# Optimization experiments

Hardware: AMD Instinct MI355X
Metric: run time of the kernel (lower is better)

Reference implementation:

```python
import jax, jax.numpy as jnp
import numpy as np

B, L, D, H, MEM, POL = 32, 256, 768, 12, 384, 3
DK = D // H
ALPHA, BETA, GAMA = 1.0, 0.25, 0.1


def _forward(sequence_output, pooled_output, adj_reshape, src_mask, aspect_mask,
             ln_g, ln_b, wq, bq, wk, bk, wd, bd, weight_m, bias_m,
             wa0, ba0, wa1, ba1, ws0, bs0, ws1, bs1, affine1, affine2, wc, bc):
    b, l, d = sequence_output.shape
    h = weight_m.shape[0]
    dk = d // h

    # custom LayerNorm (torch std is unbiased, ddof=1)
    mu = sequence_output.mean(-1, keepdims=True)
    sd = jnp.std(sequence_output, axis=-1, keepdims=True, ddof=1)
    x = ln_g * (sequence_output - mu) / (sd + 1e-6) + ln_b  # gcn_inputs (dropout = eval identity)

    aspect_outs = x * aspect_mask[:, :, None]

    # multi-head projections  [B,H,L,dk]
    q = (x @ wq + bq).reshape(b, l, h, dk).transpose(0, 2, 1, 3)
    k = (x @ wk + bk).reshape(b, l, h, dk).transpose(0, 2, 1, 3)
    asp = aspect_outs @ wd + bd                       # [B,L,dk]
    asp = jnp.broadcast_to(asp[:, None], (b, h, l, dk))

    # aspect-conditioned scores: tanh(aspect @ W_m @ K^T + b_m)   [B,H,L,L]
    asps = jnp.tanh(jnp.einsum('bhld,hde,bhme->bhlm', asp, weight_m, k) + bias_m[0])
    avg = asps.sum(axis=-2) / l                       # [B,H,L]

    # fusion overwrite: for each aspect index idx, row idx and col idx <- avg.
    # Sequential loop semantics (ascending idx, row-then-col) collapse to:
    #   both aspect (i,j): value = avg[min(i,j)];  row-only: avg[j];  col-only: avg[i]
    is_asp = aspect_mask > 0                          # [B,L]
    rowm = is_asp[:, None, :, None]
    colm = is_asp[:, None, None, :]
    avg_i = avg[..., :, None]                         # [B,H,L,1]
    avg_j = avg[..., None, :]                         # [B,H,1,L]
    ge = (jnp.arange(l)[:, None] >= jnp.arange(l)[None, :])  # i>=j -> min=j
    both_val = jnp.where(ge, avg_j, avg_i)
    aspect_scores = jnp.where(rowm & colm, both_val,
                      jnp.where(rowm, avg_j,
                        jnp.where(colm, avg_i, asps)))

    # standard scaled-dot attention
    scores = jnp.einsum('bhld,bhmd->bhlm', q, k) / jnp.sqrt(jnp.float32(dk))
    scores = jnp.where(src_mask[:, None, None, :] == 0, -1e9, scores)
    s_attn = jax.nn.softmax(scores, axis=-1)          # dropout = eval identity

    aspect_score_avg = aspect_scores.mean(axis=1)     # [B,L,L]
    adj_s = s_attn.mean(axis=1)                       # [B,L,L]

    eye = jnp.eye(l, dtype=adj_s.dtype)
    adj_s = adj_s * (1.0 - eye) + eye                 # zero diag then add identity
    adj_s = src_mask[:, :, None] * adj_s

    adj_r = jnp.exp(ALPHA * adj_reshape)
    dist_mask = aspect_score_avg > BETA
    adj_r = jnp.where(dist_mask, 1.0, adj_r)
    adj_ag = adj_r * aspect_score_avg

    log_p = jax.nn.log_softmax(adj_ag, axis=-1)
    log_q = jax.nn.log_softmax(adj_s, axis=-1)
    q_t = jnp.exp(log_q)
    kl = jnp.sum(q_t * (log_q - log_p))
    kl_loss = jnp.exp(-1.0 * kl * GAMA)

    denom_s = adj_s.sum(axis=2, keepdims=True) + 1.0
    denom_ag = adj_ag.sum(axis=2, keepdims=True) + 1.0

    out_ag, out_s = x, x
    was = [(wa0, ba0), (wa1, ba1)]
    wss = [(ws0, bs0), (ws1, bs1)]
    for li in range(2):
        g_ag = jax.nn.relu(((adj_ag @ out_ag) @ was[li][0] + was[li][1]) / denom_ag)
        g_s = jax.nn.relu(((adj_s @ out_s) @ wss[li][0] + wss[li][1]) / denom_s)
        A1 = jax.nn.softmax(jnp.einsum('bld,de,bme->blm', g_ag, affine1, g_s), axis=-1)
        A2 = jax.nn.softmax(jnp.einsum('bld,de,bme->blm', g_s, affine2, g_ag), axis=-1)
        out_ag = A1 @ g_s
        out_s = A2 @ g_ag   # gcn_drop = eval identity

    asp_wn = aspect_mask.sum(axis=1, keepdims=True)   # [B,1]
    m = aspect_mask[:, :, None]
    outputs1 = (out_ag * m).sum(axis=1) / asp_wn      # [B,MEM]
    outputs2 = (out_s * m).sum(axis=1) / asp_wn

    final = jnp.concatenate([outputs1, outputs2, pooled_output], axis=-1) @ wc + bc
    return final, kl_loss


def setup_inputs() -> dict:
    key = jax.random.key(0)
    ks = jax.random.split(key, 16)
    s = 0.02
    pos = jnp.arange(L)
    start = 5 + (jnp.arange(B) % 16)
    aspect_mask = ((pos[None, :] >= start[:, None]) & (pos[None, :] < start[:, None] + 3)).astype(jnp.float32)
    f32 = jnp.float32
    return {
        'sequence_output': jax.random.normal(ks[0], (B, L, D), f32),
        'pooled_output': jax.random.normal(ks[1], (B, D), f32),
        'adj_reshape': jax.random.uniform(ks[2], (B, L, L), f32),
        'src_mask': jnp.ones((B, L), f32),
        'aspect_mask': aspect_mask,
        'ln_g': jnp.ones((D,), f32), 'ln_b': jnp.zeros((D,), f32),
        'wq': jax.random.normal(ks[3], (D, D), f32) * s, 'bq': jnp.zeros((D,), f32),
        'wk': jax.random.normal(ks[4], (D, D), f32) * s, 'bk': jnp.zeros((D,), f32),
        'wd': jax.random.normal(ks[5], (D, DK), f32) * s, 'bd': jnp.zeros((DK,), f32),
        'weight_m': jax.random.normal(ks[6], (H, DK, DK), f32) * s,
        'bias_m': jnp.zeros((1,), f32),
        'wa0': jax.random.normal(ks[7], (D, MEM), f32) * s, 'ba0': jnp.zeros((MEM,), f32),
        'wa1': jax.random.normal(ks[8], (MEM, MEM), f32) * s, 'ba1': jnp.zeros((MEM,), f32),
        'ws0': jax.random.normal(ks[9], (D, MEM), f32) * s, 'bs0': jnp.zeros((MEM,), f32),
        'ws1': jax.random.normal(ks[10], (MEM, MEM), f32) * s, 'bs1': jnp.zeros((MEM,), f32),
        'affine1': jax.random.normal(ks[11], (MEM, MEM), f32) * s,
        'affine2': jax.random.normal(ks[12], (MEM, MEM), f32) * s,
        'wc': jax.random.normal(ks[13], (2 * D, POL), f32) * s, 'bc': jnp.zeros((POL,), f32),
    }


def reference(sequence_output, pooled_output, adj_reshape, src_mask, aspect_mask,
              ln_g, ln_b, wq, bq, wk, bk, wd, bd, weight_m, bias_m,
              wa0, ba0, wa1, ba1, ws0, bs0, ws1, bs1, affine1, affine2, wc, bc):
    return _forward(sequence_output, pooled_output, adj_reshape, src_mask, aspect_mask,
                    ln_g, ln_b, wq, bq, wk, bk, wd, bd, weight_m, bias_m,
                    wa0, ba0, wa1, ba1, ws0, bs0, ws1, bs1, affine1, affine2, wc, bc)
```

## Files before the change

### kernel.cpp

```cpp
#include <hip/hip_runtime.h>

#define B_ 32
#define L_ 256
#define D_ 768
#define H_ 12
#define DK_ 64
#define MEM_ 384

typedef __attribute__((ext_vector_type(8))) short bfrag8;
typedef __attribute__((ext_vector_type(8))) unsigned short us8;
typedef __attribute__((ext_vector_type(4))) float f32x4;

__device__ inline unsigned short f2bf(float f) {
  unsigned u = __float_as_uint(f);
  return (unsigned short)((u + 0x7fffu + ((u >> 16) & 1u)) >> 16);
}
__device__ inline float bf2f(unsigned short u) {
  return __uint_as_float(((unsigned)u) << 16);
}
__device__ inline float tanh_fast(float x) {
  x = fminf(fmaxf(x, -30.f), 30.f);
  float e = __expf(2.f * x);
  return (e - 1.f) * __builtin_amdgcn_rcpf(e + 1.f);
}
__device__ inline void gload_lds16(const unsigned short* g, unsigned short* l) {
  __builtin_amdgcn_global_load_lds(
      (__attribute__((address_space(1))) void*)(g),
      (__attribute__((address_space(3))) void*)(l), 16, 0, 0);
}

__device__ inline float waveRedSum(float v) {
#pragma unroll
  for (int o = 32; o; o >>= 1) v += __shfl_xor(v, o, 64);
  return v;
}
__device__ inline float waveRedMax(float v) {
#pragma unroll
  for (int o = 32; o; o >>= 1) v = fmaxf(v, __shfl_xor(v, o, 64));
  return v;
}
__device__ inline float blkRedSum(float v, float* red) {
  v = waveRedSum(v);
  int w = threadIdx.x >> 6;
  __syncthreads();
  if ((threadIdx.x & 63) == 0) red[w] = v;
  __syncthreads();
  return red[0] + red[1] + red[2] + red[3];
}
__device__ inline float blkRedMax(float v, float* red) {
  v = waveRedMax(v);
  int w = threadIdx.x >> 6;
  __syncthreads();
  if ((threadIdx.x & 63) == 0) red[w] = v;
  __syncthreads();
  return fmaxf(fmaxf(red[0], red[1]), fmaxf(red[2], red[3]));
}

__global__ __launch_bounds__(256) void prep_kernel(
    const float* __restrict__ seq, const float* __restrict__ lng,
    const float* __restrict__ lnb, float* __restrict__ xout,
    unsigned short* __restrict__ xbf,
    const float* __restrict__ wq, unsigned short* __restrict__ wqT,
    const float* __restrict__ wk, unsigned short* __restrict__ wkT,
    const float* __restrict__ wa0, unsigned short* __restrict__ wa0T,
    const float* __restrict__ ws0, unsigned short* __restrict__ ws0T,
    const float* __restrict__ wa1, unsigned short* __restrict__ wa1T,
    const float* __restrict__ ws1, unsigned short* __restrict__ ws1T,
    const float* __restrict__ aff1, unsigned short* __restrict__ aff1T,
    const float* __restrict__ aff2, unsigned short* __restrict__ aff2T,
    const float* __restrict__ wd, unsigned short* __restrict__ wdT,
    const float* __restrict__ wm, unsigned short* __restrict__ wmT) {
  int bid = blockIdx.x;
  if (bid >= 600) {
    long row = bid - 600;
    const float* p = seq + row * D_;
    float v[3];
#pragma unroll
    for (int i = 0; i < 3; ++i) v[i] = p[threadIdx.x + i * 256];
    __shared__ float red[4];
    float s = v[0] + v[1] + v[2];
    s = blkRedSum(s, red);
    float mu = s * (1.f / D_);
    float ss = 0.f;
#pragma unroll
    for (int i = 0; i < 3; ++i) { float d = v[i] - mu; ss += d * d; }
    ss = blkRedSum(ss, red);
    float sd = sqrtf(ss * (1.f / (D_ - 1)));
    float inv = 1.f / (sd + 1e-6f);
#pragma unroll
    for (int i = 0; i < 3; ++i) {
      int c = threadIdx.x + i * 256;
      float o = lng[c] * (v[i] - mu) * inv + lnb[c];
      xout[row * D_ + c] = o;
      xbf[row * D_ + c] = f2bf(o);
    }
    return;
  }
  const float* src; unsigned short* dst; int Rr, Cc, tIdx;
  if (bid < 144)      { src = wq;   dst = wqT;   Rr = 768; Cc = 768; tIdx = bid; }
  else if (bid < 288) { src = wk;   dst = wkT;   Rr = 768; Cc = 768; tIdx = bid - 144; }
  else if (bid < 360) { src = wa0;  dst = wa0T;  Rr = 768; Cc = 384; tIdx = bid - 288; }
  else if (bid < 432) { src = ws0;  dst = ws0T;  Rr = 768; Cc = 384; tIdx = bid - 360; }
  else if (bid < 468) { src = wa1;  dst = wa1T;  Rr = 384; Cc = 384; tIdx = bid - 432; }
  else if (bid < 504) { src = ws1;  dst = ws1T;  Rr = 384; Cc = 384; tIdx = bid - 468; }
  else if (bid < 540) { src = aff1; dst = aff1T; Rr = 384; Cc = 384; tIdx = bid - 504; }
  else if (bid < 576) { src = aff2; dst = aff2T; Rr = 384; Cc = 384; tIdx = bid - 540; }
  else if (bid < 588) { src = wd;   dst = wdT;   Rr = 768; Cc = 64;  tIdx = bid - 576; }
  else { int h = bid - 588; src = wm + h * 4096; dst = wmT + h * 4096; Rr = 64; Cc = 64; tIdx = 0; }
  __shared__ float tile[64][65];
  int nx = Cc >> 6;
  int c0 = (tIdx % nx) * 64, r0 = (tIdx / nx) * 64;
  int tx = threadIdx.x & 63, ty = threadIdx.x >> 6;
#pragma unroll
  for (int i = 0; i < 16; ++i)
    tile[ty + i * 4][tx] = src[(long)(r0 + ty + i * 4) * Cc + c0 + tx];
  __syncthreads();
#pragma unroll
  for (int i = 0; i < 16; ++i)
    dst[(long)(c0 + ty + i * 4) * Rr + r0 + tx] = f2bf(tile[tx][ty + i * 4]);
}

template <int MR>
__global__ __launch_bounds__(256) void gemm_bb(
    const unsigned short* __restrict__ A, const unsigned short* __restrict__ Bt,
    float* __restrict__ C, unsigned short* __restrict__ Cbf,
    unsigned short* __restrict__ CT,
    int M, int N, int K, long sA, long sB, long sC, long sCT,
    const float* __restrict__ bias, const float* __restrict__ rowDiv, int relu,
    const unsigned short* __restrict__ A2, const unsigned short* __restrict__ Bt2,
    float* __restrict__ C2, unsigned short* __restrict__ Cbf2,
    unsigned short* __restrict__ CT2,
    const float* __restrict__ bias2, const float* __restrict__ rowDiv2, int zsplit) {
  constexpr int MFRAG = MR / 32;
  constexpr int RW = MR / 2;
  constexpr int ASH = MR * 32;
  constexpr int BUFS = ASH + 4096;
  constexpr int TSH = 64 * (MR + 8);
  constexpr int SMN = (2 * BUFS > TSH) ? 2 * BUFS : TSH;
  __shared__ alignas(16) unsigned short smem[SMN];
  const int tid = threadIdx.x;
  const int bn = blockIdx.x, bm = blockIdx.y;
  int bz = blockIdx.z;
  const unsigned short* Ap = A; const unsigned short* Btp = Bt;
  float* Cp = C; unsigned short* Cbp = Cbf; unsigned short* CTp = CT;
  const float* biasp = bias; const float* rowDivp = rowDiv;
  if (zsplit > 0 && bz >= zsplit) {
    bz -= zsplit;
    Ap = A2; Btp = Bt2; Cp = C2; Cbp = Cbf2; CTp = CT2; biasp = bias2; rowDivp = rowDiv2;
  }
  Ap += (long)bz * sA; Btp += (long)bz * sB;
  if (Cp) Cp += (long)bz * sC;
  if (Cbp) Cbp += (long)bz * sC;
  if (CTp) CTp += (long)bz * sCT;

  f32x4 acc[MFRAG][4] = {};
  const int l = tid & 63, w = tid >> 6;
  const int wr = w >> 1, wc = w & 1;
  const int lr = l & 15, sg = l >> 4;

  const int rc = l >> 2;
  const int sslot = (l & 3) ^ ((rc >> 1) & 3);
  const unsigned short* gA0 = Ap + (long)(bm * MR + w * 16 + rc) * K + sslot * 8;
  const unsigned short* gA1 = (MR == 128)
      ? Ap + (long)(bm * MR + (w + 4) * 16 + rc) * K + sslot * 8 : nullptr;
  const unsigned short* gB0 = Btp + (long)(bn * 128 + w * 16 + rc) * K + sslot * 8;
  const unsigned short* gB1 = Btp + (long)(bn * 128 + (w + 4) * 16 + rc) * K + sslot * 8;
  const int stA0 = w * 512, stA1 = (w + 4) * 512;
  const int stB0 = ASH + w * 512, stB1 = ASH + (w + 4) * 512;

  const int swz = (sg ^ ((lr >> 1) & 3)) * 8;
  int aoff[MFRAG], boff[4];
#pragma unroll
  for (int m = 0; m < MFRAG; ++m) aoff[m] = (wr * RW + m * 16 + lr) * 32 + swz;
#pragma unroll
  for (int n = 0; n < 4; ++n) boff[n] = ASH + (wc * 64 + n * 16 + lr) * 32 + swz;

  const int nt = K >> 5;
  gload_lds16(gA0, smem + stA0);
  if (MR == 128) gload_lds16(gA1, smem + stA1);
  gload_lds16(gB0, smem + stB0);
  gload_lds16(gB1, smem + stB1);
  __syncthreads();

  for (int t = 0; t < nt; ++t) {
    const int cur = (t & 1) * BUFS;
    if (t + 1 < nt) {
      const int nxt = ((t + 1) & 1) * BUFS;
      const int k1 = (t + 1) << 5;
      gload_lds16(gA0 + k1, smem + nxt + stA0);
      if (MR == 128) gload_lds16(gA1 + k1, smem + nxt + stA1);
      gload_lds16(gB0 + k1, smem + nxt + stB0);
      gload_lds16(gB1 + k1, smem + nxt + stB1);
    }
    bfrag8 af[MFRAG], bf[4];
#pragma unroll
    for (int m = 0; m < MFRAG; ++m) af[m] = *(const bfrag8*)(smem + cur + aoff[m]);
#pragma unroll
    for (int n = 0; n < 4; ++n) bf[n] = *(const bfrag8*)(smem + cur + boff[n]);
#pragma unroll
    for (int m = 0; m < MFRAG; ++m)
#pragma unroll
      for (int n = 0; n < 4; ++n)
        acc[m][n] = __builtin_amdgcn_mfma_f32_16x16x32_bf16(af[m], bf[n], acc[m][n], 0, 0, 0);
    __syncthreads();
  }

  if (Cp || Cbp) {
#pragma unroll
    for (int m = 0; m < MFRAG; ++m) {
#pragma unroll
      for (int r = 0; r < 4; ++r) {
        int row = bm * MR + wr * RW + m * 16 + (l >> 4) * 4 + r;
        float rd = rowDivp ? 1.f / rowDivp[(long)bz * M + row] : 1.f;
#pragma unroll
        for (int n = 0; n < 4; ++n) {
          int col = bn * 128 + wc * 64 + n * 16 + lr;
          float v = acc[m][n][r];
          if (biasp) v += biasp[col];
          v *= rd;
          if (relu) v = fmaxf(v, 0.f);
          if (Cp) Cp[(long)row * N + col] = v;
          if (Cbp) Cbp[(long)row * N + col] = f2bf(v);
        }
      }
    }
  }
  if (CT) {
    auto Ts = (unsigned short(*)[MR + 8])smem;
#pragma unroll
    for (int ch = 0; ch < 2; ++ch) {
      __syncthreads();
      if (wc == ch) {
#pragma unroll
        for (int m = 0; m < MFRAG; ++m) {
#pragma unroll
          for (int r = 0; r < 4; ++r) {
            int rowl = wr * RW + m * 16 + (l >> 4) * 4 + r;
            float rd = rowDivp ? 1.f / rowDivp[(long)bz * M + bm * MR + rowl] : 1.f;
#pragma unroll
            for (int n = 0; n < 4; ++n) {
              int col = bn * 128 + wc * 64 + n * 16 + lr;
              float v = acc[m][n][r];
              if (biasp) v += biasp[col];
              v *= rd;
              if (relu) v = fmaxf(v, 0.f);
              Ts[n * 16 + lr][rowl] = f2bf(v);
            }
          }
        }
      }
      __syncthreads();
      int trow = tid >> 2, tc = (tid & 3) * (MR / 4);
      int colg = bn * 128 + ch * 64 + trow;
      int rowg = bm * MR + tc;
      unsigned short* dp = CTp + (long)(rowg >> 8) * sCT + (long)colg * 256 + (rowg & 255);
#pragma unroll
      for (int j = 0; j < MR / 32; ++j)
        *(us8*)(dp + j * 8) = *(const us8*)&Ts[trow][tc + j * 8];
    }
  }
}

__global__ __launch_bounds__(256) void attn_asp(
    const unsigned short* __restrict__ qbf, const unsigned short* __restrict__ kbf,
    const float* __restrict__ srcm,
    float* __restrict__ part0, float* __restrict__ part1,
    const unsigned short* __restrict__ xbf, const unsigned short* __restrict__ wdT,
    const float* __restrict__ amask, const float* __restrict__ bd,
    unsigned short* __restrict__ aspbf) {
  int t = threadIdx.x;
  int w = t >> 6, l = t & 63;
  int lr = l & 15, kg = (l >> 4) * 8;
  if (blockIdx.x >= 1024) {
    int l0 = (blockIdx.x - 1024) << 4;
    const unsigned short* ap = xbf + (long)(l0 + lr) * D_ + kg;
    const unsigned short* bp = wdT + (long)(w * 16 + lr) * D_ + kg;
    f32x4 acc = {};
#pragma unroll
    for (int k0 = 0; k0 < D_; k0 += 32) {
      bfrag8 af = *(const bfrag8*)(ap + k0);
      bfrag8 bf = *(const bfrag8*)(bp + k0);
      acc = __builtin_amdgcn_mfma_f32_16x16x32_bf16(af, bf, acc, 0, 0, 0);
    }
    int col = w * 16 + lr;
#pragma unroll
    for (int r = 0; r < 4; ++r) {
      int row = l0 + (l >> 4) * 4 + r;
      float v = acc[r] * amask[row] + bd[col];
      aspbf[(long)row * DK_ + col] = f2bf(v);
    }
    return;
  }
  int d = blockIdx.x;
  int b = (d & 7) + 8 * ((d >> 3) & 3);
  int rest = d >> 5;
  int l0 = (rest & 15) << 4;
  int half = rest >> 4;
  int rbase = (l >> 4) * 4;
  __shared__ float red[3][2][16][4];
  float acc[4][4] = {};
  float cmv[4];
#pragma unroll
  for (int ct = 0; ct < 4; ++ct) cmv[ct] = srcm[b * L_ + w * 64 + ct * 16 + lr];

#pragma unroll 1
  for (int ph = 0; ph < 3; ++ph) {
    int hp = half * 3 + ph;
    const unsigned short* ap = qbf + ((long)b * L_ + l0 + lr) * D_ + hp * 128 + kg;
    bfrag8 a00 = *(const bfrag8*)ap;
    bfrag8 a01 = *(const bfrag8*)(ap + 32);
    bfrag8 a10 = *(const bfrag8*)(ap + 64);
    bfrag8 a11 = *(const bfrag8*)(ap + 96);
    bfrag8 kv[4][4];
#pragma unroll
    for (int ct = 0; ct < 4; ++ct) {
      const unsigned short* bp =
          kbf + ((long)b * L_ + w * 64 + ct * 16 + lr) * D_ + hp * 128 + kg;
      kv[ct][0] = *(const bfrag8*)bp;
      kv[ct][1] = *(const bfrag8*)(bp + 32);
      kv[ct][2] = *(const bfrag8*)(bp + 64);
      kv[ct][3] = *(const bfrag8*)(bp + 96);
    }
    float sv0[4][4], sv1[4][4];
#pragma unroll
    for (int ct = 0; ct < 4; ++ct) {
      f32x4 c0 = {}, c1 = {};
      c0 = __builtin_amdgcn_mfma_f32_16x16x32_bf16(a00, kv[ct][0], c0, 0, 0, 0);
      c0 = __builtin_amdgcn_mfma_f32_16x16x32_bf16(a01, kv[ct][1], c0, 0, 0, 0);
      c1 = __builtin_amdgcn_mfma_f32_16x16x32_bf16(a10, kv[ct][2], c1, 0, 0, 0);
      c1 = __builtin_amdgcn_mfma_f32_16x16x32_bf16(a11, kv[ct][3], c1, 0, 0, 0);
      bool msk = (cmv[ct] == 0.f);
#pragma unroll
      for (int r = 0; r < 4; ++r) {
        sv0[ct][r] = __expf(msk ? -1e9f : c0[r] * 0.125f);
        sv1[ct][r] = __expf(msk ? -1e9f : c1[r] * 0.125f);
      }
    }
#pragma unroll
    for (int r = 0; r < 4; ++r) {
      float s0 = sv0[0][r] + sv0[1][r] + sv0[2][r] + sv0[3][r];
      float s1 = sv1[0][r] + sv1[1][r] + sv1[2][r] + sv1[3][r];
#pragma unroll
      for (int o = 1; o < 16; o <<= 1) {
        s0 += __shfl_xor(s0, o, 64);
        s1 += __shfl_xor(s1, o, 64);
      }
      if (lr == 0) {
        red[ph][0][rbase + r][w] = s0;
        red[ph][1][rbase + r][w] = s1;
      }
    }
    __syncthreads();
#pragma unroll
    for (int r = 0; r < 4; ++r) {
      f32x4 s4 = *(const f32x4*)&red[ph][0][rbase + r][0];
      float inv0 = __builtin_amdgcn_rcpf(s4[0] + s4[1] + s4[2] + s4[3] + 1e-30f);
      f32x4 t4 = *(const f32x4*)&red[ph][1][rbase + r][0];
      float inv1 = __builtin_amdgcn_rcpf(t4[0] + t4[1] + t4[2] + t4[3] + 1e-30f);
#pragma unroll
      for (int ct = 0; ct < 4; ++ct)
        acc[ct][r] += sv0[ct][r] * inv0 + sv1[ct][r] * inv1;
    }
  }

  float* pp = half ? part1 : part0;
#pragma unroll
  for (int r = 0; r < 4; ++r) {
    int row = l0 + rbase + r;
#pragma unroll
    for (int ct = 0; ct < 4; ++ct) {
      int col = w * 64 + ct * 16 + lr;
      pp[((long)b * L_ + row) * L_ + col] = acc[ct][r];
    }
  }
}

__global__ __launch_bounds__(256) void asp_wm_v2(const unsigned short* __restrict__ aspbf,
                                                 const unsigned short* __restrict__ wmT,
                                                 unsigned short* __restrict__ tmpA) {
  int bh = blockIdx.x;
  int b = bh / H_, h = bh % H_;
  int t = threadIdx.x;
  int w = t >> 6, l = t & 63;
  int lr = l & 15, kg = (l >> 4) * 8;
  const unsigned short* wp = wmT + h * 4096;
  f32x4 acc[4][4] = {};
#pragma unroll
  for (int ks = 0; ks < 2; ++ks) {
    int k0 = ks * 32;
    bfrag8 af[4], bf[4];
#pragma unroll
    for (int m = 0; m < 4; ++m)
      af[m] = *(const bfrag8*)(aspbf + (long)(b * L_ + w * 64 + m * 16 + lr) * DK_ + k0 + kg);
#pragma unroll
    for (int n = 0; n < 4; ++n)
      bf[n] = *(const bfrag8*)(wp + (n * 16 + lr) * 64 + k0 + kg);
#pragma unroll
    for (int m = 0; m < 4; ++m)
#pragma unroll
      for (int n = 0; n < 4; ++n)
        acc[m][n] = __builtin_amdgcn_mfma_f32_16x16x32_bf16(af[m], bf[n], acc[m][n], 0, 0, 0);
  }
#pragma unroll
  for (int m = 0; m < 4; ++m)
#pragma unroll
    for (int n = 0; n < 4; ++n)
#pragma unroll
      for (int r = 0; r < 4; ++r) {
        int row = w * 64 + m * 16 + (l >> 4) * 4 + r;
        int col = n * 16 + lr;
        tmpA[(((long)b * H_ + h) * L_ + row) * DK_ + col] = f2bf(acc[m][n][r]);
      }
}

__global__ __launch_bounds__(256) void gemm_sfmx(
    const unsigned short* __restrict__ u1, const unsigned short* __restrict__ g1,
    unsigned short* __restrict__ P1,
    const unsigned short* __restrict__ u2, const unsigned short* __restrict__ g2,
    unsigned short* __restrict__ P2) {
  constexpr int ASH = 64 * 32;
  constexpr int BUFS = ASH + 8192;
  __shared__ alignas(16) unsigned short smem[2 * BUFS];
  __shared__ float redm[2][64];
  __shared__ float reds[2][64];
  int bm = blockIdx.x;
  int bz = blockIdx.y;
  const unsigned short* Ap; const unsigned short* Bp; unsigned short* Pp;
  if (bz < 32) {
    Ap = u1 + (long)bz * L_ * MEM_; Bp = g1 + (long)bz * L_ * MEM_;
    Pp = P1 + (long)bz * L_ * L_;
  } else {
    int z = bz - 32;
    Ap = u2 + (long)z * L_ * MEM_; Bp = g2 + (long)z * L_ * MEM_;
    Pp = P2 + (long)z * L_ * L_;
  }
  const int t = threadIdx.x;
  const int l = t & 63, w = t >> 6;
  const int wr = w >> 1, wc = w & 1;
  const int lr = l & 15, sg = l >> 4;
  f32x4 acc[2][8] = {};

  const int rc = l >> 2;
  const int sslot = (l & 3) ^ ((rc >> 1) & 3);
  const unsigned short* gA = Ap + (long)(bm * 64 + w * 16 + rc) * MEM_ + sslot * 8;
  const unsigned short* gB[4];
#pragma unroll
  for (int j = 0; j < 4; ++j)
    gB[j] = Bp + (long)(w * 64 + j * 16 + rc) * MEM_ + sslot * 8;
  const int stA = w * 512;
  int stB[4];
#pragma unroll
  for (int j = 0; j < 4; ++j) stB[j] = ASH + (w * 4 + j) * 512;

  const int swz = (sg ^ ((lr >> 1) & 3)) * 8;
  int aoff[2], boff[8];
#pragma unroll
  for (int m = 0; m < 2; ++m) aoff[m] = (wr * 32 + m * 16 + lr) * 32 + swz;
#pragma unroll
  for (int n = 0; n < 8; ++n) boff[n] = ASH + (wc * 128 + n * 16 + lr) * 32 + swz;

  gload_lds16(gA, smem + stA);
#pragma unroll
  for (int j = 0; j < 4; ++j) gload_lds16(gB[j], smem + stB[j]);
  __syncthreads();

  constexpr int NT = MEM_ / 32;
  for (int tt = 0; tt < NT; ++tt) {
    const int cur = (tt & 1) * BUFS;
    if (tt + 1 < NT) {
      const int nxt = ((tt + 1) & 1) * BUFS;
      const int k1 = (tt + 1) << 5;
      gload_lds16(gA + k1, smem + nxt + stA);
#pragma unroll
      for (int j = 0; j < 4; ++j) gload_lds16(gB[j] + k1, smem + nxt + stB[j]);
    }
    bfrag8 af[2], bf[8];
#pragma unroll
    for (int m = 0; m < 2; ++m) af[m] = *(const bfrag8*)(smem + cur + aoff[m]);
#pragma unroll
    for (int n = 0; n < 8; ++n) bf[n] = *(const bfrag8*)(smem + cur + boff[n]);
#pragma unroll
    for (int m = 0; m < 2; ++m)
#pragma unroll
      for (int n = 0; n < 8; ++n)
        acc[m][n] = __builtin_amdgcn_mfma_f32_16x16x32_bf16(af[m], bf[n], acc[m][n], 0, 0, 0);
    __syncthreads();
  }

#pragma unroll
  for (int m = 0; m < 2; ++m) {
#pragma unroll
    for (int r = 0; r < 4; ++r) {
      int lrow = wr * 32 + m * 16 + (l >> 4) * 4 + r;
      float mx = -1e30f;
#pragma unroll
      for (int n = 0; n < 8; ++n) mx = fmaxf(mx, acc[m][n][r]);
#pragma unroll
      for (int o = 1; o < 16; o <<= 1) mx = fmaxf(mx, __shfl_xor(mx, o, 64));
      if (lr == 0) redm[wc][lrow] = mx;
    }
  }
  __syncthreads();
#pragma unroll
  for (int m = 0; m < 2; ++m) {
#pragma unroll
    for (int r = 0; r < 4; ++r) {
      int lrow = wr * 32 + m * 16 + (l >> 4) * 4 + r;
      float mx = fmaxf(redm[0][lrow], redm[1][lrow]);
      float s = 0.f;
#pragma unroll
      for (int n = 0; n < 8; ++n) {
        float e = __expf(acc[m][n][r] - mx);
        acc[m][n][r] = e;
        s += e;
      }
#pragma unroll
      for (int o = 1; o < 16; o <<= 1) s += __shfl_xor(s, o, 64);
      if (lr == 0) reds[wc][lrow] = s;
    }
  }
  __syncthreads();
#pragma unroll
  for (int m = 0; m < 2; ++m) {
#pragma unroll
    for (int r = 0; r < 4; ++r) {
      int lrow = wr * 32 + m * 16 + (l >> 4) * 4 + r;
      float inv = 1.f / (reds[0][lrow] + reds[1][lrow]);
      int row = bm * 64 + lrow;
#pragma unroll
      for (int n = 0; n < 8; ++n) {
        int col = wc * 128 + n * 16 + lr;
        Pp[(long)row * L_ + col] = f2bf(acc[m][n][r] * inv);
      }
    }
  }
}

__global__ __launch_bounds__(256) void asps_mean_v2(
    const unsigned short* __restrict__ tmpA,
    const unsigned short* __restrict__ kbf,
    const float* __restrict__ bias_m,
    float* __restrict__ asps_mean) {
  int blk = blockIdx.x;
  int b = blk >> 4, l0 = (blk & 15) << 4;
  int t = threadIdx.x;
  int w = t >> 6, l = t & 63;
  int lr = l & 15, kg = (l >> 4) * 8;
  float bm = bias_m[0];
  float accg[4][4] = {};
  for (int h = 0; h < H_; ++h) {
    const unsigned short* ap = tmpA + (((long)b * H_ + h) * L_ + l0 + lr) * 64 + kg;
    bfrag8 af0 = *(const bfrag8*)ap;
    bfrag8 af1 = *(const bfrag8*)(ap + 32);
#pragma unroll
    for (int ct = 0; ct < 4; ++ct) {
      const unsigned short* bp =
          kbf + ((long)b * L_ + w * 64 + ct * 16 + lr) * D_ + h * 64 + kg;
      bfrag8 bf0 = *(const bfrag8*)bp;
      bfrag8 bf1 = *(const bfrag8*)(bp + 32);
      f32x4 accl = {};
      accl = __builtin_amdgcn_mfma_f32_16x16x32_bf16(af0, bf0, accl, 0, 0, 0);
      accl = __builtin_amdgcn_mfma_f32_16x16x32_bf16(af1, bf1, accl, 0, 0, 0);
#pragma unroll
      for (int r = 0; r < 4; ++r) accg[ct][r] += tanh_fast(accl[r] + bm);
    }
  }
#pragma unroll
  for (int ct = 0; ct < 4; ++ct) {
    int col = w * 64 + ct * 16 + lr;
#pragma unroll
    for (int r = 0; r < 4; ++r) {
      int row = l0 + (l >> 4) * 4 + r;
      asps_mean[((long)b * L_ + row) * L_ + col] = accg[ct][r] * (1.f / H_);
    }
  }
}

__global__ __launch_bounds__(1024) void avgh_kernel(const float* __restrict__ asps_mean,
                                                    float* __restrict__ avgH) {
  int b = blockIdx.x;
  int m = threadIdx.x & 255, q = threadIdx.x >> 8;
  __shared__ float part[4][256];
  float s = 0.f;
  for (int l = q * 64; l < q * 64 + 64; ++l)
    s += asps_mean[((long)b * L_ + l) * L_ + m];
  part[q][m] = s;
  __syncthreads();
  if (q == 0)
    avgH[b * L_ + m] = (part[0][m] + part[1][m] + part[2][m] + part[3][m]) * (1.f / L_);
}

__global__ __launch_bounds__(256) void adjag_kl(const float* __restrict__ part0,
                                                const float* __restrict__ part1,
                                                const float* __restrict__ srcm,
                                                const float* __restrict__ asps_mean,
                                                const float* __restrict__ avgH,
                                                const float* __restrict__ amask,
                                                const float* __restrict__ adjr,
                                                unsigned short* __restrict__ adjsbf,
                                                unsigned short* __restrict__ adjagbf,
                                                float* __restrict__ klpart,
                                                float* __restrict__ den_s,
                                                float* __restrict__ den_ag) {
  long row = blockIdx.x;
  int m = threadIdx.x;
  int l = (int)(row & 255);
  int b = (int)(row >> 8);
  long idx = row * L_ + m;
  float s = (part0[idx] + part1[idx]) * (1.f / H_);
  if (m == l) s = 1.f;
  s *= srcm[b * L_ + l];
  adjsbf[idx] = f2bf(s);
  bool rowa = amask[b * L_ + l] > 0.f;
  bool cola = amask[b * L_ + m] > 0.f;
  float asa;
  if (rowa && cola) asa = (l >= m) ? avgH[b * L_ + m] : avgH[b * L_ + l];
  else if (rowa)    asa = avgH[b * L_ + m];
  else if (cola)    asa = avgH[b * L_ + l];
  else              asa = asps_mean[idx];
  float r = (asa > 0.25f) ? 1.f : expf(adjr[idx]);
  float a = r * asa;
  adjagbf[idx] = f2bf(a);

  __shared__ float red[4];
  float sum_s = blkRedSum(s, red);
  float sum_a = blkRedSum(a, red);
  float mx_s = blkRedMax(s, red);
  float mx_a = blkRedMax(a, red);
  float es = expf(s - mx_s), ea = expf(a - mx_a);
  float ses = blkRedSum(es, red);
  float sea = blkRedSum(ea, red);
  float logq = (s - mx_s) - logf(ses);
  float logp = (a - mx_a) - logf(sea);
  float term = (es / ses) * (logq - logp);
  float kp = blkRedSum(term, red);
  if (m == 0) {
    klpart[row] = kp;
    den_s[row] = sum_s + 1.f;
    den_ag[row] = sum_a + 1.f;
  }
}

__global__ __launch_bounds__(256) void final_kernel(const unsigned short* __restrict__ o_ag,
                                                    const unsigned short* __restrict__ o_s,
                                                    const float* __restrict__ pooled,
                                                    const float* __restrict__ amask,
                                                    const float* __restrict__ wc,
                                                    const float* __restrict__ bc,
                                                    const float* __restrict__ klpart,
                                                    float* __restrict__ dout) {
  int b = blockIdx.x, t = threadIdx.x;
  __shared__ float red[4];
  if (b == B_) {
    float s = 0.f;
    for (int i = t; i < B_ * L_; i += 256) s += klpart[i];
    s = blkRedSum(s, red);
    if (t == 0) dout[96] = expf(-s * 0.1f);
    return;
  }
  __shared__ float cS[1536];
  __shared__ float maskS[256];
  maskS[t] = amask[b * L_ + t];
  float wn = blkRedSum(maskS[t], red);
  for (int e = t; e < MEM_; e += 256) {
    float s1 = 0.f, s2 = 0.f;
    for (int l = 0; l < L_; ++l) {
      float mk = maskS[l];
      if (mk != 0.f) {
        s1 += mk * bf2f(o_ag[((long)b * L_ + l) * MEM_ + e]);
        s2 += mk * bf2f(o_s[((long)b * L_ + l) * MEM_ + e]);
      }
    }
    cS[e] = s1 / wn;
    cS[MEM_ + e] = s2 / wn;
  }
  for (int j = t; j < D_; j += 256) cS[2 * MEM_ + j] = pooled[b * D_ + j];
  __syncthreads();
  float p0 = 0.f, p1 = 0.f, p2 = 0.f;
  for (int j = t; j < 1536; j += 256) {
    float v = cS[j];
    p0 += v * wc[j * 3 + 0];
    p1 += v * wc[j * 3 + 1];
    p2 += v * wc[j * 3 + 2];
  }
  p0 = blkRedSum(p0, red);
  p1 = blkRedSum(p1, red);
  p2 = blkRedSum(p2, red);
  if (t == 0) {
    dout[b * 3 + 0] = p0 + bc[0];
    dout[b * 3 + 1] = p1 + bc[1];
    dout[b * 3 + 2] = p2 + bc[2];
  }
}

extern "C" void kernel_launch(void* const* d_in, const int* in_sizes, int n_in,
                              void* d_out, int out_size, void* d_ws, size_t ws_size,
                              hipStream_t stream) {
  const float* seq    = (const float*)d_in[0];
  const float* pooled = (const float*)d_in[1];
  const float* adjr   = (const float*)d_in[2];
  const float* srcm   = (const float*)d_in[3];
  const float* amask  = (const float*)d_in[4];
  const float* ln_g   = (const float*)d_in[5];
  const float* ln_b   = (const float*)d_in[6];
  const float* wq     = (const float*)d_in[7];
  const float* bq     = (const float*)d_in[8];
  const float* wk     = (const float*)d_in[9];
  const float* bk     = (const float*)d_in[10];
  const float* wd     = (const float*)d_in[11];
  const float* bd     = (const float*)d_in[12];
  const float* wm     = (const float*)d_in[13];
  const float* bm     = (const float*)d_in[14];
  const float* wa0    = (const float*)d_in[15];
  const float* ba0    = (const float*)d_in[16];
  const float* wa1    = (const float*)d_in[17];
  const float* ba1    = (const float*)d_in[18];
  const float* ws0    = (const float*)d_in[19];
  const float* bs0    = (const float*)d_in[20];
  const float* ws1    = (const float*)d_in[21];
  const float* bs1    = (const float*)d_in[22];
  const float* aff1   = (const float*)d_in[23];
  const float* aff2   = (const float*)d_in[24];
  const float* wc     = (const float*)d_in[25];
  const float* bc     = (const float*)d_in[26];

  float* ws = (float*)d_ws;
  float* S0 = ws;
  float* S1 = S0 + 6291456;
  float* S2 = S1 + 3145728;
  float* S3 = S2 + 3145728;
  float* S4 = S3 + 3145728;
  float* S5 = S4 + 524288;
  float* part0  = S5 + 2097152;
  float* part1  = part0 + 2097152;
  unsigned short* adjsbf  = (unsigned short*)(part1 + 2097152);
  unsigned short* adjagbf = adjsbf + 2097152;
  unsigned short* wT      = adjagbf + 2097152;
  unsigned short* wqT   = wT;
  unsigned short* wkT   = wT + 589824;
  unsigned short* wa0T  = wT + 1179648;
  unsigned short* ws0T  = wT + 1474560;
  unsigned short* wa1T  = wT + 1769472;
  unsigned short* ws1T  = wT + 1916928;
  unsigned short* aff1T = wT + 2064384;
  unsigned short* aff2T = wT + 2211840;
  float* tail   = (float*)(wT + 2359296);
  float* avgH   = tail;
  float* den_s  = avgH + 8192;
  float* den_ag = den_s + 8192;
  float* klp    = den_ag + 8192;

  float* x = S0;
  unsigned short* o_agbf = (unsigned short*)S0;
  unsigned short* o_sbf  = o_agbf + 3145728;
  unsigned short* gTag   = o_agbf + 6291456;
  unsigned short* gTs    = o_agbf + 9437184;
  unsigned short* xbf    = (unsigned short*)S1;
  unsigned short* qbf    = (unsigned short*)S2;
  unsigned short* tmpA   = (unsigned short*)S2;
  unsigned short* g_agbf = (unsigned short*)S2;
  unsigned short* g_sbf  = g_agbf + 3145728;
  unsigned short* kbf    = (unsigned short*)S3;
  unsigned short* tTag   = (unsigned short*)S3;
  unsigned short* tTs    = tTag + 3145728;
  unsigned short* u1bf   = (unsigned short*)S3;
  unsigned short* u2bf   = u1bf + 3145728;
  unsigned short* aspbf  = (unsigned short*)S4;
  unsigned short* wdT    = aspbf + 524288;
  unsigned short* wmT    = wdT + 49152;
  float* asps = S5;
  unsigned short* P1bf = (unsigned short*)S5;
  unsigned short* P2bf = P1bf + 2097152;
  float* dout = (float*)d_out;

  const long sAdjSh = (long)L_ * L_;
  const long sMemSh = (long)L_ * MEM_;

  prep_kernel<<<600 + B_ * L_, 256, 0, stream>>>(
      seq, ln_g, ln_b, x, xbf, wq, wqT, wk, wkT, wa0, wa0T, ws0, ws0T,
      wa1, wa1T, ws1, ws1T, aff1, aff1T, aff2, aff2T, wd, wdT, wm, wmT);
  gemm_bb<128><<<dim3(6, 64, 2), 256, 0, stream>>>(
      xbf, wqT, nullptr, qbf, nullptr, 8192, 768, 768, 0, 0, 0, 0, bq, nullptr, 0,
      xbf, wkT, nullptr, kbf, nullptr, bk, nullptr, 1);
  attn_asp<<<1536, 256, 0, stream>>>(qbf, kbf, srcm, part0, part1,
                                     xbf, wdT, amask, bd, aspbf);
  asp_wm_v2<<<B_ * H_, 256, 0, stream>>>(aspbf, wmT, tmpA);
  asps_mean_v2<<<B_ * 16, 256, 0, stream>>>(tmpA, kbf, bm, asps);
  avgh_kernel<<<B_, 1024, 0, stream>>>(asps, avgH);
  adjag_kl<<<B_ * L_, 256, 0, stream>>>(part0, part1, srcm, asps, avgH, amask, adjr,
                                        adjsbf, adjagbf, klp, den_s, den_ag);

  for (int li = 0; li < 2; ++li) {
    int Kd = li ? MEM_ : D_;
    const unsigned short* inag = li ? o_agbf : xbf;
    const unsigned short* ins  = li ? o_sbf : xbf;
    const unsigned short* wAT = li ? wa1T : wa0T;
    const float* bA = li ? ba1 : ba0;
    const unsigned short* wST = li ? ws1T : ws0T;
    const float* bS = li ? bs1 : bs0;
    gemm_bb<64><<<dim3(3, 128, 2), 256, 0, stream>>>(
        inag, wAT, nullptr, nullptr, tTag, 8192, MEM_, Kd, 0, 0, 0, sMemSh,
        nullptr, nullptr, 0,
        ins, wST, nullptr, nullptr, tTs, nullptr, nullptr, 1);
    gemm_bb<64><<<dim3(3, 4, 64), 256, 0, stream>>>(
        adjagbf, tTag, nullptr, g_agbf, gTag, L_, MEM_, L_, sAdjSh, sMemSh, sMemSh,
        sMemSh, bA, den_ag, 1,
        adjsbf, tTs, nullptr, g_sbf, gTs, bS, den_s, 32);
    gemm_bb<64><<<dim3(3, 128, 2), 256, 0, stream>>>(
        g_agbf, aff1T, nullptr, u1bf, nullptr, 8192, MEM_, MEM_, 0, 0, 0, 0,
        nullptr, nullptr, 0,
        g_sbf, aff2T, nullptr, u2bf, nullptr, nullptr, nullptr, 1);
    gemm_sfmx<<<dim3(4, 64), 256, 0, stream>>>(u1bf, g_sbf, P1bf, u2bf, g_agbf, P2bf);
    gemm_bb<64><<<dim3(3, 4, 64), 256, 0, stream>>>(
        P1bf, gTs, nullptr, o_agbf, nullptr, L_, MEM_, L_, sAdjSh, sMemSh, sMemSh, 0,
        nullptr, nullptr, 0,
        P2bf, gTag, nullptr, o_sbf, nullptr, nullptr, nullptr, 32);
  }

  final_kernel<<<B_ + 1, 256, 0, stream>>>(o_agbf, o_sbf, pooled, amask, wc, bc,
                                           klp, dout);
}
```

Before: 391.7 us.

## Overlap next-tile global loads with compute via partial vmcnt waits and prefetch

In both double-buffered GEMM loops, the full __syncthreads is replaced by an explicit s_waitcnt vmcnt(N) plus a raw s_barrier. Only the current tile's LDS loads are waited on, while the next tile's loads stay in flight during the MFMAs. In the attention-score kernel, the Q/K fragments for the next head are prefetched right after the current MFMAs, before the exp/reduction work, so their latency overlaps that work. The risks are hand-tuned vmcnt counts that must match the number of issued loads, and higher register pressure from holding the prefetched fragments.

```diff
diff --git a/kernel.cpp b/kernel.cpp
--- a/kernel.cpp
+++ b/kernel.cpp
@@ -180,7 +180,6 @@
   if (MR == 128) gload_lds16(gA1, smem + stA1);
   gload_lds16(gB0, smem + stB0);
   gload_lds16(gB1, smem + stB1);
-  __syncthreads();
 
   for (int t = 0; t < nt; ++t) {
     const int cur = (t & 1) * BUFS;
@@ -191,7 +190,15 @@
       if (MR == 128) gload_lds16(gA1 + k1, smem + nxt + stA1);
       gload_lds16(gB0 + k1, smem + nxt + stB0);
       gload_lds16(gB1 + k1, smem + nxt + stB1);
-    }
+      if constexpr (MR == 128)
+        asm volatile("s_waitcnt vmcnt(4)" ::: "memory");
+      else
+        asm volatile("s_waitcnt vmcnt(3)" ::: "memory");
+    } else {
+      asm volatile("s_waitcnt vmcnt(0)" ::: "memory");
+    }
+    __builtin_amdgcn_s_barrier();
+    asm volatile("" ::: "memory");
     bfrag8 af[MFRAG], bf[4];
 #pragma unroll
     for (int m = 0; m < MFRAG; ++m) af[m] = *(const bfrag8*)(smem + cur + aoff[m]);
@@ -202,7 +209,9 @@
 #pragma unroll
       for (int n = 0; n < 4; ++n)
         acc[m][n] = __builtin_amdgcn_mfma_f32_16x16x32_bf16(af[m], bf[n], acc[m][n], 0, 0, 0);
-    __syncthreads();
+    asm volatile("" ::: "memory");
+    __builtin_amdgcn_s_barrier();
+    asm volatile("" ::: "memory");
   }
 
   if (Cp || Cbp) {
@@ -303,24 +312,26 @@
 #pragma unroll
   for (int ct = 0; ct < 4; ++ct) cmv[ct] = srcm[b * L_ + w * 64 + ct * 16 + lr];
 
+  const int hp0 = half * 3;
+  const long qrow = (long)b * L_ + l0 + lr;
+  const unsigned short* apq = qbf + qrow * D_ + hp0 * 128 + kg;
+  bfrag8 a00 = *(const bfrag8*)apq;
+  bfrag8 a01 = *(const bfrag8*)(apq + 32);
+  bfrag8 a10 = *(const bfrag8*)(apq + 64);
+  bfrag8 a11 = *(const bfrag8*)(apq + 96);
+  bfrag8 kv[4][4];
+#pragma unroll
+  for (int ct = 0; ct < 4; ++ct) {
+    const unsigned short* bp =
+        kbf + ((long)b * L_ + w * 64 + ct * 16 + lr) * D_ + hp0 * 128 + kg;
+    kv[ct][0] = *(const bfrag8*)bp;
+    kv[ct][1] = *(const bfrag8*)(bp + 32);
+    kv[ct][2] = *(const bfrag8*)(bp + 64);
+    kv[ct][3] = *(const bfrag8*)(bp + 96);
+  }
+
 #pragma unroll 1
   for (int ph = 0; ph < 3; ++ph) {
-    int hp = half * 3 + ph;
-    const unsigned short* ap = qbf + ((long)b * L_ + l0 + lr) * D_ + hp * 128 + kg;
-    bfrag8 a00 = *(const bfrag8*)ap;
-    bfrag8 a01 = *(const bfrag8*)(ap + 32);
-    bfrag8 a10 = *(const bfrag8*)(ap + 64);
-    bfrag8 a11 = *(const bfrag8*)(ap + 96);
-    bfrag8 kv[4][4];
-#pragma unroll
-    for (int ct = 0; ct < 4; ++ct) {
-      const unsigned short* bp =
-          kbf + ((long)b * L_ + w * 64 + ct * 16 + lr) * D_ + hp * 128 + kg;
-      kv[ct][0] = *(const bfrag8*)bp;
-      kv[ct][1] = *(const bfrag8*)(bp + 32);
-      kv[ct][2] = *(const bfrag8*)(bp + 64);
-      kv[ct][3] = *(const bfrag8*)(bp + 96);
-    }
     float sv0[4][4], sv1[4][4];
 #pragma unroll
     for (int ct = 0; ct < 4; ++ct) {
@@ -329,11 +340,32 @@
       c0 = __builtin_amdgcn_mfma_f32_16x16x32_bf16(a01, kv[ct][1], c0, 0, 0, 0);
       c1 = __builtin_amdgcn_mfma_f32_16x16x32_bf16(a10, kv[ct][2], c1, 0, 0, 0);
       c1 = __builtin_amdgcn_mfma_f32_16x16x32_bf16(a11, kv[ct][3], c1, 0, 0, 0);
+#pragma unroll
+      for (int r = 0; r < 4; ++r) { sv0[ct][r] = c0[r]; sv1[ct][r] = c1[r]; }
+    }
+    if (ph < 2) {
+      const unsigned short* apn = qbf + qrow * D_ + (hp0 + ph + 1) * 128 + kg;
+      a00 = *(const bfrag8*)apn;
+      a01 = *(const bfrag8*)(apn + 32);
+      a10 = *(const bfrag8*)(apn + 64);
+      a11 = *(const bfrag8*)(apn + 96);
+#pragma unroll
+      for (int ct = 0; ct < 4; ++ct) {
+        const unsigned short* bp =
+            kbf + ((long)b * L_ + w * 64 + ct * 16 + lr) * D_ + (hp0 + ph + 1) * 128 + kg;
+        kv[ct][0] = *(const bfrag8*)bp;
+        kv[ct][1] = *(const bfrag8*)(bp + 32);
+        kv[ct][2] = *(const bfrag8*)(bp + 64);
+        kv[ct][3] = *(const bfrag8*)(bp + 96);
+      }
+    }
+#pragma unroll
+    for (int ct = 0; ct < 4; ++ct) {
       bool msk = (cmv[ct] == 0.f);
 #pragma unroll
       for (int r = 0; r < 4; ++r) {
-        sv0[ct][r] = __expf(msk ? -1e9f : c0[r] * 0.125f);
-        sv1[ct][r] = __expf(msk ? -1e9f : c1[r] * 0.125f);
+        sv0[ct][r] = __expf(msk ? -1e9f : sv0[ct][r] * 0.125f);
+        sv1[ct][r] = __expf(msk ? -1e9f : sv1[ct][r] * 0.125f);
       }
     }
 #pragma unroll
@@ -462,7 +494,6 @@
   gload_lds16(gA, smem + stA);
 #pragma unroll
   for (int j = 0; j < 4; ++j) gload_lds16(gB[j], smem + stB[j]);
-  __syncthreads();
 
   constexpr int NT = MEM_ / 32;
   for (int tt = 0; tt < NT; ++tt) {
@@ -473,7 +504,12 @@
       gload_lds16(gA + k1, smem + nxt + stA);
 #pragma unroll
       for (int j = 0; j < 4; ++j) gload_lds16(gB[j] + k1, smem + nxt + stB[j]);
-    }
+      asm volatile("s_waitcnt vmcnt(5)" ::: "memory");
+    } else {
+      asm volatile("s_waitcnt vmcnt(0)" ::: "memory");
+    }
+    __builtin_amdgcn_s_barrier();
+    asm volatile("" ::: "memory");
     bfrag8 af[2], bf[8];
 #pragma unroll
     for (int m = 0; m < 2; ++m) af[m] = *(const bfrag8*)(smem + cur + aoff[m]);
@@ -484,7 +520,9 @@
 #pragma unroll
       for (int n = 0; n < 8; ++n)
         acc[m][n] = __builtin_amdgcn_mfma_f32_16x16x32_bf16(af[m], bf[n], acc[m][n], 0, 0, 0);
-    __syncthreads();
+    asm volatile("" ::: "memory");
+    __builtin_amdgcn_s_barrier();
+    asm volatile("" ::: "memory");
   }
 
 #pragma unroll
```

Measured after the change: 390.0 us. Within noise of the previous version (-0.4%).
